# Performance work log

Measured on AMD Instinct MI355X. Metric: run time of the kernel, lower is better.

## Reference

```python
import jax, jax.numpy as jnp
import numpy as np

N_NODES = 50000
N_EDGES = 400000
IN_F = 512
HID = 512      # 2 * out_features
OUT_F = 256
N_CELL = 1000
N_DIM = 128
N_SEL = 8192
N_C = 1024


def setup_inputs() -> dict:
    key = jax.random.key(0)
    ks = jax.random.split(key, 16)
    x = jax.random.normal(ks[0], (N_NODES, IN_F), dtype=jnp.float32)
    src = jax.random.randint(ks[1], (N_EDGES,), 0, N_NODES, dtype=jnp.int32)
    dst = jax.random.randint(ks[2], (N_EDGES,), 0, N_NODES, dtype=jnp.int32)
    x_indices = jax.random.randint(ks[3], (N_SEL,), 0, N_NODES, dtype=jnp.int32)
    c_indices = jax.random.randint(ks[4], (N_C,), 0, N_CELL, dtype=jnp.int32)
    s = lambda f: 1.0 / np.sqrt(f)
    W1 = jax.random.normal(ks[5], (IN_F, HID), dtype=jnp.float32) * s(IN_F)
    b1 = jnp.zeros((HID,), jnp.float32)
    W2 = jax.random.normal(ks[6], (HID, HID), dtype=jnp.float32) * s(HID)
    b2 = jnp.zeros((HID,), jnp.float32)
    W3 = jax.random.normal(ks[7], (HID, OUT_F), dtype=jnp.float32) * s(HID)
    b3 = jnp.zeros((OUT_F,), jnp.float32)
    Wp = jax.random.normal(ks[8], (OUT_F, N_DIM), dtype=jnp.float32) * s(OUT_F)
    bp = jnp.zeros((N_DIM,), jnp.float32)
    emb = jax.random.normal(ks[9], (N_CELL, N_DIM), dtype=jnp.float32)
    return {"x": x, "src": src, "dst": dst, "x_indices": x_indices,
            "c_indices": c_indices, "W1": W1, "b1": b1, "W2": W2, "b2": b2,
            "W3": W3, "b3": b3, "Wp": Wp, "bp": bp, "emb": emb}


def _degree_norms(src, dst, n):
    ones = jnp.ones(src.shape[0], jnp.float32)
    deg_out = jax.ops.segment_sum(ones, src, num_segments=n)
    deg_in = jax.ops.segment_sum(ones, dst, num_segments=n)
    ns = jnp.where(deg_out > 0, jax.lax.rsqrt(jnp.maximum(deg_out, 1.0)), 0.0)
    nd = jnp.where(deg_in > 0, jax.lax.rsqrt(jnp.maximum(deg_in, 1.0)), 0.0)
    return ns[:, None], nd[:, None]


def _gconv(h, src, dst, norm_src, norm_dst, W, b, n):
    # DGL GraphConv, norm='both': D_in^{-1/2} A D_out^{-1/2} H W + b
    msg = (h * norm_src)[src]                         # [E, F]
    agg = jax.ops.segment_sum(msg, dst, num_segments=n)
    return (agg * norm_dst) @ W + b


def reference(x, src, dst, x_indices, c_indices, W1, b1, W2, b2, W3, b3, Wp, bp, emb):
    n = x.shape[0]
    ns, nd = _degree_norms(src, dst, n)
    h = jax.nn.relu(_gconv(x, src, dst, ns, nd, W1, b1, n))
    h = jax.nn.relu(_gconv(h, src, dst, ns, nd, W2, b2, n))
    h = jax.nn.relu(_gconv(h, src, dst, ns, nd, W3, b3, n))
    enc = h[x_indices]                                # [N_SEL, OUT_F]
    proj = enc @ Wp + bp                              # Dropout in eval mode = identity
    e = emb[c_indices]                                # [N_C, N_DIM]
    return e @ proj.T                                 # [N_C, N_SEL]
```

## Files before the change

### kernel.cpp

```cpp
#include <hip/hip_runtime.h>

typedef unsigned int u32;
typedef unsigned short u16;

#define N_NODES 50000
#define N_EDGES 400000
#define IN_F 512
#define HID 512
#define OUT_F 256
#define N_CELL 1000
#define N_DIM 128
#define N_SEL 8192
#define N_C 1024
#define MPAD 50048

#define SCAN_B 256
#define SCAN_NB ((N_NODES + SCAN_B - 1) / SCAN_B)

typedef __bf16 bf16x8 __attribute__((ext_vector_type(8)));
typedef float f32x4 __attribute__((ext_vector_type(4)));

__device__ __forceinline__ u16 f2bf(float f) {
    u32 u = __builtin_bit_cast(u32, f);
    u32 r = (u + 0x7fffu + ((u >> 16) & 1u)) >> 16;
    return (u16)r;
}
__device__ __forceinline__ float bf2f(u32 bits16) {
    return __builtin_bit_cast(float, bits16 << 16);
}

__device__ __forceinline__ void async_copy16(const u16* g, u16* l) {
    __builtin_amdgcn_global_load_lds(
        (const __attribute__((address_space(1))) void*)g,
        (__attribute__((address_space(3))) void*)l, 16, 0, 0);
}


__global__ void degrees_kernel(const int* __restrict__ src, const int* __restrict__ dst,
                               int* __restrict__ degO, int* __restrict__ degI) {
    int e = blockIdx.x * 256 + threadIdx.x;
    if (e < N_EDGES) {
        atomicAdd(&degO[src[e]], 1);
        atomicAdd(&degI[dst[e]], 1);
    }
}

__global__ void scan_blocksum_kernel(const int* __restrict__ deg, int* __restrict__ bsum) {
    __shared__ int sh[SCAN_B];
    int i = blockIdx.x * SCAN_B + threadIdx.x;
    int v = (i < N_NODES) ? deg[i] : 0;
    sh[threadIdx.x] = v;
    __syncthreads();
    for (int off = SCAN_B / 2; off > 0; off >>= 1) {
        if (threadIdx.x < off) sh[threadIdx.x] += sh[threadIdx.x + off];
        __syncthreads();
    }
    if (threadIdx.x == 0) bsum[blockIdx.x] = sh[0];
}

__global__ void scan_bsum_kernel(const int* __restrict__ bsum, int* __restrict__ boff) {
    __shared__ int sh[SCAN_B];
    const int t = threadIdx.x;
    int v = (t < SCAN_NB) ? bsum[t] : 0;
    sh[t] = v;
    __syncthreads();
    for (int off = 1; off < SCAN_B; off <<= 1) {
        int u = (t >= off) ? sh[t - off] : 0;
        __syncthreads();
        sh[t] += u;
        __syncthreads();
    }
    if (t < SCAN_NB) boff[t] = sh[t] - v;
}

__global__ void scan_final_kernel(const int* __restrict__ deg, const int* __restrict__ boff,
                                  int* __restrict__ offs) {
    __shared__ int sh[SCAN_B];
    const int t = threadIdx.x;
    int i = blockIdx.x * SCAN_B + t;
    int v = (i < N_NODES) ? deg[i] : 0;
    sh[t] = v;
    __syncthreads();
    for (int off = 1; off < SCAN_B; off <<= 1) {
        int u = (t >= off) ? sh[t - off] : 0;
        __syncthreads();
        sh[t] += u;
        __syncthreads();
    }
    if (i < N_NODES) offs[i] = boff[blockIdx.x] + sh[t] - v;
    if (i == 0) offs[N_NODES] = N_EDGES;
}

__global__ void fill_csr_kernel(const int* __restrict__ src, const int* __restrict__ dst,
                                int* __restrict__ cursor, const int* __restrict__ offs,
                                int* __restrict__ csr) {
    int e = blockIdx.x * 256 + threadIdx.x;
    if (e < N_EDGES) {
        int d = dst[e];
        int slot = atomicAdd(&cursor[d], 1);
        csr[offs[d] + slot] = src[e];
    }
}

__global__ void norms_kernel(const int* __restrict__ degO, const int* __restrict__ degI,
                             float* __restrict__ ns, float* __restrict__ nd) {
    int i = blockIdx.x * 256 + threadIdx.x;
    if (i < N_NODES) {
        ns[i] = degO[i] > 0 ? rsqrtf((float)degO[i]) : 0.f;
        nd[i] = degI[i] > 0 ? rsqrtf((float)degI[i]) : 0.f;
    }
}


__global__ void trans_bf16_kernel(const float* __restrict__ src, u16* __restrict__ dst,
                                  int K, int N) {
    int i = blockIdx.x * 256 + threadIdx.x;
    if (i >= K * N) return;
    int n = i / K, k = i % K;
    dst[i] = f2bf(src[k * N + n]);
}

__global__ void convert_x_kernel(const float* __restrict__ x, u16* __restrict__ xb) {
    int i = blockIdx.x * 256 + threadIdx.x;
    int base = i * 4;
    int m = base >> 9;
    ushort4 o;
    if (m < N_NODES) {
        float4 v = *(const float4*)(x + base);
        o.x = f2bf(v.x); o.y = f2bf(v.y); o.z = f2bf(v.z); o.w = f2bf(v.w);
    } else {
        o = make_ushort4(0, 0, 0, 0);
    }
    *(ushort4*)(xb + base) = o;
}

__global__ void gather_emb_kernel(const float* __restrict__ emb, const int* __restrict__ cidx,
                                  u16* __restrict__ eb) {
    int c = blockIdx.x, f = threadIdx.x;
    eb[c * N_DIM + f] = f2bf(emb[(size_t)cidx[c] * N_DIM + f]);
}

__global__ __launch_bounds__(256, 2) void gemm_bf16_nt(
    const u16* __restrict__ A, const u16* __restrict__ B,
    const int* __restrict__ aidx,
    u16* __restrict__ Cb, float* __restrict__ Cf,
    const float* __restrict__ scale, int nScale,
    const float* __restrict__ bias,
    int N, int K) {
    __shared__ __align__(16) u16 As[128 * 32];
    __shared__ __align__(16) u16 Bs[128 * 32];
    const int t = threadIdx.x;
    const int m0 = blockIdx.x * 128, n0 = blockIdx.y * 128;
    const int l = t & 63, w = t >> 6;
    const int wm = (w >> 1) << 6, wn = (w & 1) << 6;
    const int lr = l & 15, quad = l >> 4;

    const int lrow = l >> 2;
    const int kof = (l & 3) << 3;
    const int r0 = w, r1 = w + 4;
    int ar0 = m0 + r0 * 16 + lrow;
    int ar1 = m0 + r1 * 16 + lrow;
    if (aidx) { ar0 = aidx[ar0]; ar1 = aidx[ar1]; }
    const u16* gA0 = A + (size_t)ar0 * K + kof;
    const u16* gA1 = A + (size_t)ar1 * K + kof;
    const u16* gB0 = B + (size_t)(n0 + r0 * 16 + lrow) * K + kof;
    const u16* gB1 = B + (size_t)(n0 + r1 * 16 + lrow) * K + kof;
    u16* lA0 = As + r0 * 512;
    u16* lA1 = As + r1 * 512;
    u16* lB0 = Bs + r0 * 512;
    u16* lB1 = Bs + r1 * 512;

    f32x4 acc[4][4] = {};

    for (int ks = 0; ks < K; ks += 32) {
        async_copy16(gA0 + ks, lA0);
        async_copy16(gA1 + ks, lA1);
        async_copy16(gB0 + ks, lB0);
        async_copy16(gB1 + ks, lB1);
        __syncthreads();
        bf16x8 af[4], bg[4];
#pragma unroll
        for (int i = 0; i < 4; ++i)
            af[i] = *(const bf16x8*)&As[(wm + i * 16 + lr) * 32 + quad * 8];
#pragma unroll
        for (int j = 0; j < 4; ++j)
            bg[j] = *(const bf16x8*)&Bs[(wn + j * 16 + lr) * 32 + quad * 8];
#pragma unroll
        for (int i = 0; i < 4; ++i)
#pragma unroll
            for (int j = 0; j < 4; ++j)
                acc[i][j] = __builtin_amdgcn_mfma_f32_16x16x32_bf16(af[i], bg[j], acc[i][j], 0, 0, 0);
        __syncthreads();
    }

#pragma unroll
    for (int i = 0; i < 4; ++i) {
        int rbase = m0 + wm + i * 16 + quad * 4;
#pragma unroll
        for (int j = 0; j < 4; ++j) {
            int col = n0 + wn + j * 16 + lr;
            float bv = bias ? bias[col] : 0.f;
#pragma unroll
            for (int r = 0; r < 4; ++r) {
                int rg = rbase + r;
                float sc = scale ? (rg < nScale ? scale[rg] : 0.f) : 1.f;
                float v = acc[i][j][r] * sc + bv;
                if (Cb) Cb[(size_t)rg * N + col] = f2bf(v);
                else    Cf[(size_t)rg * N + col] = v;
            }
        }
    }
}

template <int W32>
struct AggVec;
template <> struct AggVec<4> { using T = uint4; };
template <> struct AggVec<2> { using T = uint2; };

template <int F>
__global__ __launch_bounds__(256) void aggregate_kernel(
    const u16* __restrict__ T, const int* __restrict__ csr,
    const int* __restrict__ offs, const float* __restrict__ nd,
    const float* __restrict__ bias, u16* __restrict__ H) {
    constexpr int W32 = F / 128;
    using VT = typename AggVec<W32>::T;
    const int t = threadIdx.x, w = t >> 6, l = t & 63;
    const int node = blockIdx.x * 4 + w;
    u32* __restrict__ Hrow = (u32*)H + (size_t)node * (F / 2) + l * W32;
    if (node >= N_NODES) {
        VT z = {};
        *(VT*)Hrow = z;
        return;
    }
    const int s0 = __builtin_amdgcn_readfirstlane(offs[node]);
    const int s1 = __builtin_amdgcn_readfirstlane(offs[node + 1]);
    const u32* __restrict__ Tb = (const u32*)T + l * W32;

    float acc[4][2 * W32];
#pragma unroll
    for (int c = 0; c < 4; ++c)
#pragma unroll
        for (int j = 0; j < 2 * W32; ++j) acc[c][j] = 0.f;

    int e = s0;
    for (; e + 4 <= s1; e += 4) {
        int si[4];
#pragma unroll
        for (int c = 0; c < 4; ++c) si[c] = csr[e + c];
        VT v[4];
#pragma unroll
        for (int c = 0; c < 4; ++c)
            v[c] = *(const VT*)(Tb + (size_t)si[c] * (F / 2));
#pragma unroll
        for (int c = 0; c < 4; ++c) {
            const u32* vv = (const u32*)&v[c];
#pragma unroll
            for (int j = 0; j < W32; ++j) {
                acc[c][2 * j] += bf2f(vv[j] & 0xffffu);
                acc[c][2 * j + 1] += bf2f(vv[j] >> 16);
            }
        }
    }
    for (; e < s1; ++e) {
        int s = csr[e];
        VT v = *(const VT*)(Tb + (size_t)s * (F / 2));
        const u32* vv = (const u32*)&v;
#pragma unroll
        for (int j = 0; j < W32; ++j) {
            acc[0][2 * j] += bf2f(vv[j] & 0xffffu);
            acc[0][2 * j + 1] += bf2f(vv[j] >> 16);
        }
    }

    const float ndv = nd[node];
    u32 ow[W32];
#pragma unroll
    for (int j = 0; j < W32; ++j) {
        float a0 = acc[0][2 * j] + acc[1][2 * j] + acc[2][2 * j] + acc[3][2 * j];
        float a1 = acc[0][2 * j + 1] + acc[1][2 * j + 1] + acc[2][2 * j + 1] + acc[3][2 * j + 1];
        float r0 = fmaxf(fmaf(a0, ndv, bias[l * 2 * W32 + 2 * j]), 0.f);
        float r1 = fmaxf(fmaf(a1, ndv, bias[l * 2 * W32 + 2 * j + 1]), 0.f);
        ow[j] = (u32)f2bf(r0) | ((u32)f2bf(r1) << 16);
    }
    VT o;
    u32* op = (u32*)&o;
#pragma unroll
    for (int j = 0; j < W32; ++j) op[j] = ow[j];
    *(VT*)Hrow = o;
}


extern "C" void kernel_launch(void* const* d_in, const int* in_sizes, int n_in,
                              void* d_out, int out_size, void* d_ws, size_t ws_size,
                              hipStream_t stream) {
    const float* x   = (const float*)d_in[0];
    const int*   src = (const int*)d_in[1];
    const int*   dst = (const int*)d_in[2];
    const int*   xidx= (const int*)d_in[3];
    const int*   cidx= (const int*)d_in[4];
    const float* W1  = (const float*)d_in[5];
    const float* b1  = (const float*)d_in[6];
    const float* W2  = (const float*)d_in[7];
    const float* b2  = (const float*)d_in[8];
    const float* W3  = (const float*)d_in[9];
    const float* b3  = (const float*)d_in[10];
    const float* Wp  = (const float*)d_in[11];
    const float* bp  = (const float*)d_in[12];
    const float* emb = (const float*)d_in[13];
    float* out = (float*)d_out;

    char* p = (char*)d_ws;
    auto alloc = [&](size_t bytes) {
        char* r = p;
        p += (bytes + 255) & ~(size_t)255;
        return r;
    };
    u16* T    = (u16*)alloc((size_t)MPAD * 512 * 2);
    u16* HX   = (u16*)alloc((size_t)MPAD * 512 * 2);
    u16* W1T  = (u16*)alloc((size_t)512 * 512 * 2);
    u16* W2T  = (u16*)alloc((size_t)512 * 512 * 2);
    u16* W3T  = (u16*)alloc((size_t)256 * 512 * 2);
    u16* WpT  = (u16*)alloc((size_t)128 * 256 * 2);
    u16* projb= (u16*)alloc((size_t)N_SEL * N_DIM * 2);
    u16* eb   = (u16*)alloc((size_t)N_C * N_DIM * 2);
    int* degO   = (int*)alloc(N_NODES * 4);
    int* degI   = (int*)alloc(N_NODES * 4);
    int* cursor = (int*)alloc(N_NODES * 4);
    int* offs   = (int*)alloc((N_NODES + 1) * 4);
    float* ns   = (float*)alloc(N_NODES * 4);
    float* nd   = (float*)alloc(N_NODES * 4);
    int* csr    = (int*)alloc(N_EDGES * 4);
    int* bsum   = (int*)alloc(SCAN_NB * 4);
    int* boff   = (int*)alloc(SCAN_NB * 4);
    if ((size_t)(p - (char*)d_ws) > ws_size) return;

    hipMemsetAsync(degO, 0, (size_t)((char*)offs - (char*)degO), stream);
    degrees_kernel<<<(N_EDGES + 255) / 256, 256, 0, stream>>>(src, dst, degO, degI);
    scan_blocksum_kernel<<<SCAN_NB, SCAN_B, 0, stream>>>(degI, bsum);
    scan_bsum_kernel<<<1, SCAN_B, 0, stream>>>(bsum, boff);
    scan_final_kernel<<<SCAN_NB, SCAN_B, 0, stream>>>(degI, boff, offs);
    fill_csr_kernel<<<(N_EDGES + 255) / 256, 256, 0, stream>>>(src, dst, cursor, offs, csr);
    norms_kernel<<<(N_NODES + 255) / 256, 256, 0, stream>>>(degO, degI, ns, nd);

    trans_bf16_kernel<<<(512 * 512) / 256, 256, 0, stream>>>(W1, W1T, 512, 512);
    trans_bf16_kernel<<<(512 * 512) / 256, 256, 0, stream>>>(W2, W2T, 512, 512);
    trans_bf16_kernel<<<(512 * 256) / 256, 256, 0, stream>>>(W3, W3T, 512, 256);
    trans_bf16_kernel<<<(256 * 128) / 256, 256, 0, stream>>>(Wp, WpT, 256, 128);
    convert_x_kernel<<<(MPAD * 512 / 4) / 256, 256, 0, stream>>>(x, HX);
    gather_emb_kernel<<<N_C, N_DIM, 0, stream>>>(emb, cidx, eb);

    gemm_bf16_nt<<<dim3(MPAD / 128, 512 / 128), 256, 0, stream>>>(
        HX, W1T, nullptr, T, nullptr, ns, N_NODES, nullptr, 512, 512);
    aggregate_kernel<512><<<MPAD / 4, 256, 0, stream>>>(T, csr, offs, nd, b1, HX);
    gemm_bf16_nt<<<dim3(MPAD / 128, 512 / 128), 256, 0, stream>>>(
        HX, W2T, nullptr, T, nullptr, ns, N_NODES, nullptr, 512, 512);
    aggregate_kernel<512><<<MPAD / 4, 256, 0, stream>>>(T, csr, offs, nd, b2, HX);
    gemm_bf16_nt<<<dim3(MPAD / 128, 256 / 128), 256, 0, stream>>>(
        HX, W3T, nullptr, T, nullptr, ns, N_NODES, nullptr, 256, 512);
    aggregate_kernel<256><<<MPAD / 4, 256, 0, stream>>>(T, csr, offs, nd, b3, HX);

    gemm_bf16_nt<<<dim3(N_SEL / 128, 1), 256, 0, stream>>>(
        HX, WpT, xidx, projb, nullptr, nullptr, 0, bp, N_DIM, 256);
    gemm_bf16_nt<<<dim3(N_C / 128, N_SEL / 128), 256, 0, stream>>>(
        eb, projb, nullptr, nullptr, out, nullptr, 0, nullptr, N_SEL, N_DIM);
}
```

Baseline: 612.7 us.

## Enlarge GEMM tile to 256x128 with 8 waves and unroll aggregation by 8

The GEMM block grows from 128x128 with 4 waves to 256x128 with 8 waves. Each thread now issues two A copies and one B copy, so the B tile is reused across twice as many rows. MPAD is raised to 50176 so it divides evenly by 256. The aggregation kernel gains an 8-edge unrolled loop to keep more gathers in flight. The larger block uses more LDS and registers per block, and launch_bounds(512,4) may force register spilling.

```diff
diff --git a/kernel.cpp b/kernel.cpp
--- a/kernel.cpp
+++ b/kernel.cpp
@@ -12,7 +12,7 @@
 #define N_DIM 128
 #define N_SEL 8192
 #define N_C 1024
-#define MPAD 50048
+#define MPAD 50176
 
 #define SCAN_B 256
 #define SCAN_NB ((N_NODES + SCAN_B - 1) / SCAN_B)
@@ -140,35 +140,33 @@
     eb[c * N_DIM + f] = f2bf(emb[(size_t)cidx[c] * N_DIM + f]);
 }
 
-__global__ __launch_bounds__(256, 2) void gemm_bf16_nt(
+__global__ __launch_bounds__(512, 4) void gemm_bf16_nt(
     const u16* __restrict__ A, const u16* __restrict__ B,
     const int* __restrict__ aidx,
     u16* __restrict__ Cb, float* __restrict__ Cf,
     const float* __restrict__ scale, int nScale,
     const float* __restrict__ bias,
     int N, int K) {
-    __shared__ __align__(16) u16 As[128 * 32];
+    __shared__ __align__(16) u16 As[256 * 32];
     __shared__ __align__(16) u16 Bs[128 * 32];
     const int t = threadIdx.x;
-    const int m0 = blockIdx.x * 128, n0 = blockIdx.y * 128;
+    const int m0 = blockIdx.x * 256, n0 = blockIdx.y * 128;
     const int l = t & 63, w = t >> 6;
-    const int wm = (w >> 1) << 6, wn = (w & 1) << 6;
+    const int wm = (w >> 1) << 6;
+    const int wn = (w & 1) << 6;
     const int lr = l & 15, quad = l >> 4;
 
     const int lrow = l >> 2;
     const int kof = (l & 3) << 3;
-    const int r0 = w, r1 = w + 4;
-    int ar0 = m0 + r0 * 16 + lrow;
-    int ar1 = m0 + r1 * 16 + lrow;
+    int ar0 = m0 + w * 16 + lrow;
+    int ar1 = m0 + (w + 8) * 16 + lrow;
     if (aidx) { ar0 = aidx[ar0]; ar1 = aidx[ar1]; }
     const u16* gA0 = A + (size_t)ar0 * K + kof;
     const u16* gA1 = A + (size_t)ar1 * K + kof;
-    const u16* gB0 = B + (size_t)(n0 + r0 * 16 + lrow) * K + kof;
-    const u16* gB1 = B + (size_t)(n0 + r1 * 16 + lrow) * K + kof;
-    u16* lA0 = As + r0 * 512;
-    u16* lA1 = As + r1 * 512;
-    u16* lB0 = Bs + r0 * 512;
-    u16* lB1 = Bs + r1 * 512;
+    const u16* gB0 = B + (size_t)(n0 + w * 16 + lrow) * K + kof;
+    u16* lA0 = As + w * 512;
+    u16* lA1 = As + (w + 8) * 512;
+    u16* lB0 = Bs + w * 512;
 
     f32x4 acc[4][4] = {};
 
@@ -176,7 +174,6 @@
         async_copy16(gA0 + ks, lA0);
         async_copy16(gA1 + ks, lA1);
         async_copy16(gB0 + ks, lB0);
-        async_copy16(gB1 + ks, lB1);
         __syncthreads();
         bf16x8 af[4], bg[4];
 #pragma unroll
@@ -243,6 +240,24 @@
         for (int j = 0; j < 2 * W32; ++j) acc[c][j] = 0.f;
 
     int e = s0;
+    for (; e + 8 <= s1; e += 8) {
+        int si[8];
+#pragma unroll
+        for (int c = 0; c < 8; ++c) si[c] = csr[e + c];
+        VT v[8];
+#pragma unroll
+        for (int c = 0; c < 8; ++c)
+            v[c] = *(const VT*)(Tb + (size_t)si[c] * (F / 2));
+#pragma unroll
+        for (int c = 0; c < 8; ++c) {
+            const u32* vv = (const u32*)&v[c];
+#pragma unroll
+            for (int j = 0; j < W32; ++j) {
+                acc[c & 3][2 * j] += bf2f(vv[j] & 0xffffu);
+                acc[c & 3][2 * j + 1] += bf2f(vv[j] >> 16);
+            }
+        }
+    }
     for (; e + 4 <= s1; e += 4) {
         int si[4];
 #pragma unroll
@@ -349,18 +364,18 @@
     convert_x_kernel<<<(MPAD * 512 / 4) / 256, 256, 0, stream>>>(x, HX);
     gather_emb_kernel<<<N_C, N_DIM, 0, stream>>>(emb, cidx, eb);
 
-    gemm_bf16_nt<<<dim3(MPAD / 128, 512 / 128), 256, 0, stream>>>(
+    gemm_bf16_nt<<<dim3(MPAD / 256, 512 / 128), 512, 0, stream>>>(
         HX, W1T, nullptr, T, nullptr, ns, N_NODES, nullptr, 512, 512);
     aggregate_kernel<512><<<MPAD / 4, 256, 0, stream>>>(T, csr, offs, nd, b1, HX);
-    gemm_bf16_nt<<<dim3(MPAD / 128, 512 / 128), 256, 0, stream>>>(
+    gemm_bf16_nt<<<dim3(MPAD / 256, 512 / 128), 512, 0, stream>>>(
         HX, W2T, nullptr, T, nullptr, ns, N_NODES, nullptr, 512, 512);
     aggregate_kernel<512><<<MPAD / 4, 256, 0, stream>>>(T, csr, offs, nd, b2, HX);
-    gemm_bf16_nt<<<dim3(MPAD / 128, 256 / 128), 256, 0, stream>>>(
+    gemm_bf16_nt<<<dim3(MPAD / 256, 256 / 128), 512, 0, stream>>>(
         HX, W3T, nullptr, T, nullptr, ns, N_NODES, nullptr, 256, 512);
     aggregate_kernel<256><<<MPAD / 4, 256, 0, stream>>>(T, csr, offs, nd, b3, HX);
 
-    gemm_bf16_nt<<<dim3(N_SEL / 128, 1), 256, 0, stream>>>(
+    gemm_bf16_nt<<<dim3(N_SEL / 256, 1), 512, 0, stream>>>(
         HX, WpT, xidx, projb, nullptr, nullptr, 0, bp, N_DIM, 256);
-    gemm_bf16_nt<<<dim3(N_C / 128, N_SEL / 128), 256, 0, stream>>>(
+    gemm_bf16_nt<<<dim3(N_C / 256, N_SEL / 128), 512, 0, stream>>>(
         eb, projb, nullptr, nullptr, out, nullptr, 0, nullptr, N_SEL, N_DIM);
 }
```

Result: no change. 612.6 us (-0.0%).

## Double-buffer GEMM LDS tiles and unroll gather-aggregate loop by eight

Applied to the files above, without the earlier changes.

The bf16 GEMM now uses two LDS buffers per operand and prefetches the next K-slice with async global-to-LDS copies while the current slice runs on MFMA, leaving one barrier per iteration instead of two. The CSR aggregation kernel gains an 8-edge unrolled loop so more row gathers are in flight before the accumulates. MPAD grows to a multiple of 256 rows, presumably to match padding needs elsewhere. The costs are doubled LDS use per block, which can limit occupancy, and higher register pressure in the aggregation kernel.

```diff
diff --git a/kernel.cpp b/kernel.cpp
--- a/kernel.cpp
+++ b/kernel.cpp
@@ -12,7 +12,7 @@
 #define N_DIM 128
 #define N_SEL 8192
 #define N_C 1024
-#define MPAD 50048
+#define MPAD 50176
 
 #define SCAN_B 256
 #define SCAN_NB ((N_NODES + SCAN_B - 1) / SCAN_B)
@@ -147,8 +147,8 @@
     const float* __restrict__ scale, int nScale,
     const float* __restrict__ bias,
     int N, int K) {
-    __shared__ __align__(16) u16 As[128 * 32];
-    __shared__ __align__(16) u16 Bs[128 * 32];
+    __shared__ __align__(16) u16 As[2 * 4096];
+    __shared__ __align__(16) u16 Bs[2 * 4096];
     const int t = threadIdx.x;
     const int m0 = blockIdx.x * 128, n0 = blockIdx.y * 128;
     const int l = t & 63, w = t >> 6;
@@ -172,25 +172,35 @@
 
     f32x4 acc[4][4] = {};
 
-    for (int ks = 0; ks < K; ks += 32) {
-        async_copy16(gA0 + ks, lA0);
-        async_copy16(gA1 + ks, lA1);
-        async_copy16(gB0 + ks, lB0);
-        async_copy16(gB1 + ks, lB1);
-        __syncthreads();
+    async_copy16(gA0, lA0);
+    async_copy16(gA1, lA1);
+    async_copy16(gB0, lB0);
+    async_copy16(gB1, lB1);
+
+    const int niter = K >> 5;
+    for (int it = 0; it < niter; ++it) {
+        const int cur = (it & 1) << 12;
+        const int nxt = 4096 - cur;
+        __syncthreads();
+        if (it + 1 < niter) {
+            const int ks = (it + 1) << 5;
+            async_copy16(gA0 + ks, lA0 + nxt);
+            async_copy16(gA1 + ks, lA1 + nxt);
+            async_copy16(gB0 + ks, lB0 + nxt);
+            async_copy16(gB1 + ks, lB1 + nxt);
+        }
         bf16x8 af[4], bg[4];
 #pragma unroll
         for (int i = 0; i < 4; ++i)
-            af[i] = *(const bf16x8*)&As[(wm + i * 16 + lr) * 32 + quad * 8];
+            af[i] = *(const bf16x8*)&As[cur + (wm + i * 16 + lr) * 32 + quad * 8];
 #pragma unroll
         for (int j = 0; j < 4; ++j)
-            bg[j] = *(const bf16x8*)&Bs[(wn + j * 16 + lr) * 32 + quad * 8];
+            bg[j] = *(const bf16x8*)&Bs[cur + (wn + j * 16 + lr) * 32 + quad * 8];
 #pragma unroll
         for (int i = 0; i < 4; ++i)
 #pragma unroll
             for (int j = 0; j < 4; ++j)
                 acc[i][j] = __builtin_amdgcn_mfma_f32_16x16x32_bf16(af[i], bg[j], acc[i][j], 0, 0, 0);
-        __syncthreads();
     }
 
 #pragma unroll
@@ -243,6 +253,24 @@
         for (int j = 0; j < 2 * W32; ++j) acc[c][j] = 0.f;
 
     int e = s0;
+    for (; e + 8 <= s1; e += 8) {
+        int si[8];
+#pragma unroll
+        for (int c = 0; c < 8; ++c) si[c] = csr[e + c];
+        VT v[8];
+#pragma unroll
+        for (int c = 0; c < 8; ++c)
+            v[c] = *(const VT*)(Tb + (size_t)si[c] * (F / 2));
+#pragma unroll
+        for (int c = 0; c < 8; ++c) {
+            const u32* vv = (const u32*)&v[c];
+#pragma unroll
+            for (int j = 0; j < W32; ++j) {
+                acc[c & 3][2 * j] += bf2f(vv[j] & 0xffffu);
+                acc[c & 3][2 * j + 1] += bf2f(vv[j] >> 16);
+            }
+        }
+    }
     for (; e + 4 <= s1; e += 4) {
         int si[4];
 #pragma unroll
```

After: 601.0 us. Within noise of the previous version (-1.9%).
